# Performance work log

Hardware: AMD Instinct MI355X
Metric: run time of the kernel (lower is better)

Reference implementation:

```python
import jax, jax.numpy as jnp
import numpy as np

EPS = 1e-5
TOP_K = 2


def setup_inputs() -> dict:
    key = jax.random.key(0)
    ks = jax.random.split(key, 6)
    T, H, F, E = 4096, 1024, 2816, 8
    scale = 0.02
    return {
        "hidden_states": jax.random.normal(ks[0], (T, H), dtype=jnp.float32),
        "ln_w": jnp.ones((H,), dtype=jnp.float32),
        "router_w": jax.random.normal(ks[1], (H, E), dtype=jnp.float32) * scale,
        "w_gate": jax.random.normal(ks[2], (E, H, F), dtype=jnp.float32) * scale,
        "w_up": jax.random.normal(ks[3], (E, H, F), dtype=jnp.float32) * scale,
        "w_down": jax.random.normal(ks[4], (E, F, H), dtype=jnp.float32) * scale,
    }


def reference(hidden_states, ln_w, router_w, w_gate, w_up, w_down):
    # RMSNorm (LlamaRMSNorm)
    var = jnp.mean(hidden_states * hidden_states, axis=-1, keepdims=True)
    x = hidden_states * jax.lax.rsqrt(var + EPS) * ln_w  # [T, H]

    # TopKRouter: softmax over experts, then top-k probs/indices
    logits = x @ router_w                     # [T, E]
    probs = jax.nn.softmax(logits, axis=-1)
    topk_p, topk_i = jax.lax.top_k(probs, TOP_K)  # [T, K]

    # Dense combine weights [T, E]: prob for routed experts, 0 otherwise
    T = x.shape[0]
    combine = jnp.zeros_like(probs).at[jnp.arange(T)[:, None], topk_i].add(topk_p)

    # Experts: Llama-style gated MLP (SwiGLU); loop over fixed small expert set
    out = jnp.zeros_like(x)
    for e in range(w_gate.shape[0]):
        h = jax.nn.silu(x @ w_gate[e]) * (x @ w_up[e])   # [T, F]
        out = out + combine[:, e:e + 1] * (h @ w_down[e])
    return out
```

## Files before the change

kernel.cpp:

```cpp
#include <hip/hip_runtime.h>

#define T_TOK 4096
#define H_DIM 1024
#define F_DIM 2816
#define E_NUM 8
#define EPSV 1e-5f

typedef unsigned short u16;
typedef __attribute__((ext_vector_type(8))) short bf16x8;
typedef __attribute__((ext_vector_type(4))) float f32x4;

__device__ __forceinline__ u16 f2bf(float f) {
  union { float f; unsigned u; } c; c.f = f;
  unsigned u = c.u;
  return (u16)((u + 0x7FFFu + ((u >> 16) & 1u)) >> 16);
}

__global__ __launch_bounds__(256) void router_kernel(
    const float* __restrict__ hs, const float* __restrict__ lnw,
    const float* __restrict__ rw, u16* __restrict__ x_h,
    int* __restrict__ cnt, int* __restrict__ list,
    float* __restrict__ wcomb, int* __restrict__ slot) {
  const int wave = threadIdx.x >> 6;
  const int lane = threadIdx.x & 63;
  const int t = blockIdx.x * 4 + wave;
  const float* row = hs + (size_t)t * H_DIM;

  float4 v[4];
  float ss = 0.f;
#pragma unroll
  for (int j = 0; j < 4; ++j) {
    v[j] = ((const float4*)row)[j * 64 + lane];
    ss += v[j].x * v[j].x + v[j].y * v[j].y + v[j].z * v[j].z + v[j].w * v[j].w;
  }
#pragma unroll
  for (int m = 32; m; m >>= 1) ss += __shfl_xor(ss, m, 64);
  const float inv = rsqrtf(ss * (1.0f / H_DIM) + EPSV);

  float lg[E_NUM];
#pragma unroll
  for (int e = 0; e < E_NUM; ++e) lg[e] = 0.f;

#pragma unroll
  for (int j = 0; j < 4; ++j) {
    const int idx = j * 64 + lane;
    const int h0 = idx * 4;
    float4 w4 = ((const float4*)lnw)[idx];
    float xv[4] = {v[j].x * inv * w4.x, v[j].y * inv * w4.y,
                   v[j].z * inv * w4.z, v[j].w * inv * w4.w};
    ushort4 xs;
    xs.x = f2bf(xv[0]); xs.y = f2bf(xv[1]); xs.z = f2bf(xv[2]); xs.w = f2bf(xv[3]);
    ((ushort4*)(x_h + (size_t)t * H_DIM))[idx] = xs;
#pragma unroll
    for (int q = 0; q < 4; ++q) {
      const float* rr = rw + (size_t)(h0 + q) * E_NUM;
      float4 a = ((const float4*)rr)[0];
      float4 b = ((const float4*)rr)[1];
      lg[0] += xv[q] * a.x; lg[1] += xv[q] * a.y;
      lg[2] += xv[q] * a.z; lg[3] += xv[q] * a.w;
      lg[4] += xv[q] * b.x; lg[5] += xv[q] * b.y;
      lg[6] += xv[q] * b.z; lg[7] += xv[q] * b.w;
    }
  }
#pragma unroll
  for (int e = 0; e < E_NUM; ++e)
#pragma unroll
    for (int m = 32; m; m >>= 1) lg[e] += __shfl_xor(lg[e], m, 64);

  if (lane == 0) {
    float mx = lg[0];
#pragma unroll
    for (int e = 1; e < E_NUM; ++e) mx = fmaxf(mx, lg[e]);
    float p[E_NUM], s = 0.f;
#pragma unroll
    for (int e = 0; e < E_NUM; ++e) { p[e] = __expf(lg[e] - mx); s += p[e]; }
    const float invs = 1.0f / s;
    int e1 = 0; float b1 = p[0];
#pragma unroll
    for (int e = 1; e < E_NUM; ++e) if (p[e] > b1) { b1 = p[e]; e1 = e; }
    int e2 = -1; float b2 = -1.f;
#pragma unroll
    for (int e = 0; e < E_NUM; ++e) if (e != e1 && p[e] > b2) { b2 = p[e]; e2 = e; }
    b1 *= invs; b2 *= invs;
    int p1 = atomicAdd(&cnt[e1], 1);
    list[e1 * T_TOK + p1] = t; wcomb[e1 * T_TOK + p1] = b1;
    slot[2 * t] = (e1 << 16) | p1;
    int p2 = atomicAdd(&cnt[e2], 1);
    list[e2 * T_TOK + p2] = t; wcomb[e2 * T_TOK + p2] = b2;
    slot[2 * t + 1] = (e2 << 16) | p2;
  }
}

__global__ void offsets_kernel(const int* __restrict__ cnt, int* __restrict__ offs) {
  if (threadIdx.x == 0) {
    int s = 0;
    for (int e = 0; e < E_NUM; ++e) { offs[e] = s; s += cnt[e]; }
  }
}

__global__ __launch_bounds__(256) void transpose_cvt(
    const float* __restrict__ in, u16* __restrict__ out, int R, int C) {
  __shared__ float tile[32][33];
  const size_t base = (size_t)blockIdx.z * R * C;
  const int c0 = blockIdx.x * 32, r0 = blockIdx.y * 32;
  const int tx = threadIdx.x, ty = threadIdx.y;
#pragma unroll
  for (int j = 0; j < 32; j += 8)
    tile[ty + j][tx] = in[base + (size_t)(r0 + ty + j) * C + c0 + tx];
  __syncthreads();
#pragma unroll
  for (int j = 0; j < 32; j += 8)
    out[base + (size_t)(c0 + ty + j) * R + r0 + tx] = f2bf(tile[tx][ty + j]);
}

__global__ __launch_bounds__(256) void gemm1_kernel(
    const u16* __restrict__ x_h, const u16* __restrict__ wgT,
    const u16* __restrict__ wuT, const int* __restrict__ cnt,
    const int* __restrict__ offs, const int* __restrict__ list,
    u16* __restrict__ hbuf) {
  const int e = blockIdx.z;
  const int n_e = cnt[e];
  const int rt = blockIdx.y;
  if (rt * 128 >= n_e) return;
  const int ft = blockIdx.x;

  __shared__ __align__(16) u16 As[128][72];
  __shared__ __align__(16) u16 Bgs[64][72];
  __shared__ __align__(16) u16 Bus[64][72];
  __shared__ int tok[128];

  const int tid = threadIdx.x;
  if (tid < 128) {
    int r = rt * 128 + tid;
    if (r >= n_e) r = n_e - 1;
    tok[tid] = list[e * T_TOK + r];
  }
  __syncthreads();

  const int wv = tid >> 6, lane = tid & 63;
  const int wm = wv >> 1, wn = wv & 1;
  const int lrow = lane & 15, quad = lane >> 4;

  f32x4 accg[4][2], accu[4][2];
#pragma unroll
  for (int i = 0; i < 4; ++i)
#pragma unroll
    for (int j = 0; j < 2; ++j) {
      accg[i][j] = f32x4{0.f, 0.f, 0.f, 0.f};
      accu[i][j] = f32x4{0.f, 0.f, 0.f, 0.f};
    }

  const size_t wb = ((size_t)e * F_DIM + (size_t)ft * 64) * H_DIM;

  for (int k0 = 0; k0 < H_DIM; k0 += 64) {
#pragma unroll
    for (int i = 0; i < 4; ++i) {
      int c = tid + i * 256;
      int r = c >> 3, kc = (c & 7) << 3;
      *(uint4*)&As[r][kc] = *(const uint4*)(x_h + (size_t)tok[r] * H_DIM + k0 + kc);
    }
#pragma unroll
    for (int i = 0; i < 2; ++i) {
      int c = tid + i * 256;
      int fr = c >> 3, kc = (c & 7) << 3;
      size_t g = wb + (size_t)fr * H_DIM + k0 + kc;
      *(uint4*)&Bgs[fr][kc] = *(const uint4*)(wgT + g);
      *(uint4*)&Bus[fr][kc] = *(const uint4*)(wuT + g);
    }
    __syncthreads();
#pragma unroll
    for (int ks = 0; ks < 2; ++ks) {
      const int kk = ks * 32 + quad * 8;
      bf16x8 a[4], bg[2], bu[2];
#pragma unroll
      for (int tm = 0; tm < 4; ++tm)
        a[tm] = *(const bf16x8*)&As[wm * 64 + tm * 16 + lrow][kk];
#pragma unroll
      for (int tn = 0; tn < 2; ++tn) {
        bg[tn] = *(const bf16x8*)&Bgs[wn * 32 + tn * 16 + lrow][kk];
        bu[tn] = *(const bf16x8*)&Bus[wn * 32 + tn * 16 + lrow][kk];
      }
#pragma unroll
      for (int tm = 0; tm < 4; ++tm)
#pragma unroll
        for (int tn = 0; tn < 2; ++tn) {
          accg[tm][tn] = __builtin_amdgcn_mfma_f32_16x16x32_bf16(a[tm], bg[tn], accg[tm][tn], 0, 0, 0);
          accu[tm][tn] = __builtin_amdgcn_mfma_f32_16x16x32_bf16(a[tm], bu[tn], accu[tm][tn], 0, 0, 0);
        }
    }
    __syncthreads();
  }

  const int oe = offs[e];
#pragma unroll
  for (int tm = 0; tm < 4; ++tm) {
    const int lr0 = wm * 64 + tm * 16 + quad * 4;
#pragma unroll
    for (int rr = 0; rr < 4; ++rr) {
      const int gr = rt * 128 + lr0 + rr;
      if (gr < n_e) {
#pragma unroll
        for (int tn = 0; tn < 2; ++tn) {
          float g = accg[tm][tn][rr];
          float u = accu[tm][tn][rr];
          float hv = g / (1.0f + __expf(-g)) * u;
          int col = ft * 64 + wn * 32 + tn * 16 + lrow;
          hbuf[(size_t)(oe + gr) * F_DIM + col] = f2bf(hv);
        }
      }
    }
  }
}

__global__ __launch_bounds__(256) void gemm2_kernel(
    const u16* __restrict__ hbuf, const u16* __restrict__ wdT,
    const int* __restrict__ cnt, const int* __restrict__ offs,
    const float* __restrict__ wcomb, float* __restrict__ contrib) {
  const int e = blockIdx.z;
  const int n_e = cnt[e];
  const int rt = blockIdx.y;
  if (rt * 128 >= n_e) return;
  const int nt = blockIdx.x;

  __shared__ __align__(16) u16 As[128][72];
  __shared__ __align__(16) u16 Bs[64][72];
  __shared__ int hrow[128];

  const int tid = threadIdx.x;
  const int oe = offs[e];
  if (tid < 128) {
    int r = rt * 128 + tid;
    if (r >= n_e) r = n_e - 1;
    hrow[tid] = oe + r;
  }
  __syncthreads();

  const int wv = tid >> 6, lane = tid & 63;
  const int wm = wv >> 1, wn = wv & 1;
  const int lrow = lane & 15, quad = lane >> 4;

  f32x4 acc[4][2];
#pragma unroll
  for (int i = 0; i < 4; ++i)
#pragma unroll
    for (int j = 0; j < 2; ++j) acc[i][j] = f32x4{0.f, 0.f, 0.f, 0.f};

  const size_t wb = ((size_t)e * H_DIM + (size_t)nt * 64) * F_DIM;

  for (int k0 = 0; k0 < F_DIM; k0 += 64) {
#pragma unroll
    for (int i = 0; i < 4; ++i) {
      int c = tid + i * 256;
      int r = c >> 3, kc = (c & 7) << 3;
      *(uint4*)&As[r][kc] = *(const uint4*)(hbuf + (size_t)hrow[r] * F_DIM + k0 + kc);
    }
#pragma unroll
    for (int i = 0; i < 2; ++i) {
      int c = tid + i * 256;
      int fr = c >> 3, kc = (c & 7) << 3;
      *(uint4*)&Bs[fr][kc] = *(const uint4*)(wdT + wb + (size_t)fr * F_DIM + k0 + kc);
    }
    __syncthreads();
#pragma unroll
    for (int ks = 0; ks < 2; ++ks) {
      const int kk = ks * 32 + quad * 8;
      bf16x8 a[4], b[2];
#pragma unroll
      for (int tm = 0; tm < 4; ++tm)
        a[tm] = *(const bf16x8*)&As[wm * 64 + tm * 16 + lrow][kk];
#pragma unroll
      for (int tn = 0; tn < 2; ++tn)
        b[tn] = *(const bf16x8*)&Bs[wn * 32 + tn * 16 + lrow][kk];
#pragma unroll
      for (int tm = 0; tm < 4; ++tm)
#pragma unroll
        for (int tn = 0; tn < 2; ++tn)
          acc[tm][tn] = __builtin_amdgcn_mfma_f32_16x16x32_bf16(a[tm], b[tn], acc[tm][tn], 0, 0, 0);
    }
    __syncthreads();
  }

#pragma unroll
  for (int tm = 0; tm < 4; ++tm) {
    const int lr0 = wm * 64 + tm * 16 + quad * 4;
#pragma unroll
    for (int rr = 0; rr < 4; ++rr) {
      const int gr = rt * 128 + lr0 + rr;
      if (gr < n_e) {
        const float cw = wcomb[e * T_TOK + gr];
#pragma unroll
        for (int tn = 0; tn < 2; ++tn) {
          int col = nt * 64 + wn * 32 + tn * 16 + lrow;
          contrib[(size_t)(oe + gr) * H_DIM + col] = acc[tm][tn][rr] * cw;
        }
      }
    }
  }
}

__global__ __launch_bounds__(256) void combine_kernel(
    const float* __restrict__ contrib, const int* __restrict__ offs,
    const int* __restrict__ slot, float* __restrict__ out) {
  const int t = blockIdx.x;
  const int s0 = slot[2 * t], s1 = slot[2 * t + 1];
  const int r0 = offs[s0 >> 16] + (s0 & 0xFFFF);
  const int r1 = offs[s1 >> 16] + (s1 & 0xFFFF);
  float4 a = ((const float4*)(contrib + (size_t)r0 * H_DIM))[threadIdx.x];
  float4 b = ((const float4*)(contrib + (size_t)r1 * H_DIM))[threadIdx.x];
  float4 o = {a.x + b.x, a.y + b.y, a.z + b.z, a.w + b.w};
  ((float4*)(out + (size_t)t * H_DIM))[threadIdx.x] = o;
}

extern "C" void kernel_launch(void* const* d_in, const int* in_sizes, int n_in,
                              void* d_out, int out_size, void* d_ws, size_t ws_size,
                              hipStream_t stream) {
  const float* hs  = (const float*)d_in[0];
  const float* lnw = (const float*)d_in[1];
  const float* rw  = (const float*)d_in[2];
  const float* wg  = (const float*)d_in[3];
  const float* wu  = (const float*)d_in[4];
  const float* wd  = (const float*)d_in[5];
  float* out = (float*)d_out;

  char* p = (char*)d_ws;
  const size_t SZ_XH = (size_t)T_TOK * H_DIM * 2;
  const size_t SZ_W  = (size_t)E_NUM * F_DIM * H_DIM * 2;
  const size_t SZ_HB = (size_t)T_TOK * 2 * F_DIM * 2;
  const size_t SZ_CT = (size_t)T_TOK * 2 * H_DIM * 4;

  u16* x_h  = (u16*)p;   p += SZ_XH;
  u16* wgT  = (u16*)p;   p += SZ_W;
  u16* wuT  = (u16*)p;   p += SZ_W;
  u16* wdT  = (u16*)p;   p += SZ_W;
  u16* hbuf = (u16*)p;   p += SZ_HB;
  float* contrib = (float*)p; p += SZ_CT;
  int* cnt  = (int*)p;   p += 256;
  int* offs = (int*)p;   p += 256;
  int* list = (int*)p;   p += (size_t)E_NUM * T_TOK * 4;
  float* wcomb = (float*)p; p += (size_t)E_NUM * T_TOK * 4;
  int* slot = (int*)p;   p += (size_t)T_TOK * 2 * 4;

  hipMemsetAsync(cnt, 0, 256, stream);
  router_kernel<<<T_TOK / 4, 256, 0, stream>>>(hs, lnw, rw, x_h, cnt, list, wcomb, slot);
  offsets_kernel<<<1, 64, 0, stream>>>(cnt, offs);
  transpose_cvt<<<dim3(F_DIM / 32, H_DIM / 32, E_NUM), dim3(32, 8), 0, stream>>>(wg, wgT, H_DIM, F_DIM);
  transpose_cvt<<<dim3(F_DIM / 32, H_DIM / 32, E_NUM), dim3(32, 8), 0, stream>>>(wu, wuT, H_DIM, F_DIM);
  transpose_cvt<<<dim3(H_DIM / 32, F_DIM / 32, E_NUM), dim3(32, 8), 0, stream>>>(wd, wdT, F_DIM, H_DIM);
  gemm1_kernel<<<dim3(F_DIM / 64, T_TOK / 128, E_NUM), 256, 0, stream>>>(x_h, wgT, wuT, cnt, offs, list, hbuf);
  gemm2_kernel<<<dim3(H_DIM / 64, T_TOK / 128, E_NUM), 256, 0, stream>>>(hbuf, wdT, cnt, offs, wcomb, contrib);
  combine_kernel<<<T_TOK, 256, 0, stream>>>(contrib, offs, slot, out);
}
```

Before: 673.6 us.

## Use direct global-to-LDS loads with XOR swizzle and widen gemm2 N tile

Result: faster. 654.4 us (-2.9%).

```diff
diff --git a/kernel.cpp b/kernel.cpp
--- a/kernel.cpp
+++ b/kernel.cpp
@@ -14,6 +14,12 @@
   union { float f; unsigned u; } c; c.f = f;
   unsigned u = c.u;
   return (u16)((u + 0x7FFFu + ((u >> 16) & 1u)) >> 16);
+}
+
+__device__ __forceinline__ void llds16(const u16* g, u16* l) {
+  __builtin_amdgcn_global_load_lds(
+      (const __attribute__((address_space(1))) unsigned int*)g,
+      (__attribute__((address_space(3))) unsigned int*)l, 16, 0, 0);
 }
 
 __global__ __launch_bounds__(256) void router_kernel(
@@ -124,9 +130,9 @@
   if (rt * 128 >= n_e) return;
   const int ft = blockIdx.x;
 
-  __shared__ __align__(16) u16 As[128][72];
-  __shared__ __align__(16) u16 Bgs[64][72];
-  __shared__ __align__(16) u16 Bus[64][72];
+  __shared__ __align__(16) u16 As[128 * 64];
+  __shared__ __align__(16) u16 Bgs[64 * 64];
+  __shared__ __align__(16) u16 Bus[64 * 64];
   __shared__ int tok[128];
 
   const int tid = threadIdx.x;
@@ -140,6 +146,42 @@
   const int wv = tid >> 6, lane = tid & 63;
   const int wm = wv >> 1, wn = wv & 1;
   const int lrow = lane & 15, quad = lane >> 4;
+  const int srow = lane >> 3, schunk = lane & 7;
+
+  const u16* agp[4];
+#pragma unroll
+  for (int i = 0; i < 4; ++i) {
+    int r = wv * 32 + i * 8 + srow;
+    agp[i] = x_h + (size_t)tok[r] * H_DIM + ((schunk ^ (r & 7)) << 3);
+  }
+  const size_t wb = ((size_t)e * F_DIM + (size_t)ft * 64) * H_DIM;
+  const u16* bgp[2]; const u16* bup[2];
+#pragma unroll
+  for (int i = 0; i < 2; ++i) {
+    int r = wv * 16 + i * 8 + srow;
+    size_t g = wb + (size_t)r * H_DIM + ((schunk ^ (r & 7)) << 3);
+    bgp[i] = wgT + g;
+    bup[i] = wuT + g;
+  }
+
+  const u16* aptr[4][2]; const u16* bgptr[2][2]; const u16* buptr[2][2];
+#pragma unroll
+  for (int tm = 0; tm < 4; ++tm) {
+    int row = wm * 64 + tm * 16 + lrow;
+#pragma unroll
+    for (int ks = 0; ks < 2; ++ks)
+      aptr[tm][ks] = &As[row * 64 + (((ks * 4 + quad) ^ (row & 7)) << 3)];
+  }
+#pragma unroll
+  for (int tn = 0; tn < 2; ++tn) {
+    int row = wn * 32 + tn * 16 + lrow;
+#pragma unroll
+    for (int ks = 0; ks < 2; ++ks) {
+      int off = row * 64 + (((ks * 4 + quad) ^ (row & 7)) << 3);
+      bgptr[tn][ks] = &Bgs[off];
+      buptr[tn][ks] = &Bus[off];
+    }
+  }
 
   f32x4 accg[4][2], accu[4][2];
 #pragma unroll
@@ -150,35 +192,25 @@
       accu[i][j] = f32x4{0.f, 0.f, 0.f, 0.f};
     }
 
-  const size_t wb = ((size_t)e * F_DIM + (size_t)ft * 64) * H_DIM;
-
   for (int k0 = 0; k0 < H_DIM; k0 += 64) {
 #pragma unroll
-    for (int i = 0; i < 4; ++i) {
-      int c = tid + i * 256;
-      int r = c >> 3, kc = (c & 7) << 3;
-      *(uint4*)&As[r][kc] = *(const uint4*)(x_h + (size_t)tok[r] * H_DIM + k0 + kc);
-    }
+    for (int i = 0; i < 4; ++i)
+      llds16(agp[i] + k0, &As[(wv * 32 + i * 8) * 64]);
 #pragma unroll
     for (int i = 0; i < 2; ++i) {
-      int c = tid + i * 256;
-      int fr = c >> 3, kc = (c & 7) << 3;
-      size_t g = wb + (size_t)fr * H_DIM + k0 + kc;
-      *(uint4*)&Bgs[fr][kc] = *(const uint4*)(wgT + g);
-      *(uint4*)&Bus[fr][kc] = *(const uint4*)(wuT + g);
+      llds16(bgp[i] + k0, &Bgs[(wv * 16 + i * 8) * 64]);
+      llds16(bup[i] + k0, &Bus[(wv * 16 + i * 8) * 64]);
     }
     __syncthreads();
 #pragma unroll
     for (int ks = 0; ks < 2; ++ks) {
-      const int kk = ks * 32 + quad * 8;
       bf16x8 a[4], bg[2], bu[2];
 #pragma unroll
-      for (int tm = 0; tm < 4; ++tm)
-        a[tm] = *(const bf16x8*)&As[wm * 64 + tm * 16 + lrow][kk];
+      for (int tm = 0; tm < 4; ++tm) a[tm] = *(const bf16x8*)aptr[tm][ks];
 #pragma unroll
       for (int tn = 0; tn < 2; ++tn) {
-        bg[tn] = *(const bf16x8*)&Bgs[wn * 32 + tn * 16 + lrow][kk];
-        bu[tn] = *(const bf16x8*)&Bus[wn * 32 + tn * 16 + lrow][kk];
+        bg[tn] = *(const bf16x8*)bgptr[tn][ks];
+        bu[tn] = *(const bf16x8*)buptr[tn][ks];
       }
 #pragma unroll
       for (int tm = 0; tm < 4; ++tm)
@@ -222,8 +254,8 @@
   if (rt * 128 >= n_e) return;
   const int nt = blockIdx.x;
 
-  __shared__ __align__(16) u16 As[128][72];
-  __shared__ __align__(16) u16 Bs[64][72];
+  __shared__ __align__(16) u16 As[128 * 64];
+  __shared__ __align__(16) u16 Bs[128 * 64];
   __shared__ int hrow[128];
 
   const int tid = threadIdx.x;
@@ -238,43 +270,62 @@
   const int wv = tid >> 6, lane = tid & 63;
   const int wm = wv >> 1, wn = wv & 1;
   const int lrow = lane & 15, quad = lane >> 4;
-
-  f32x4 acc[4][2];
+  const int srow = lane >> 3, schunk = lane & 7;
+
+  const u16* agp[4];
+#pragma unroll
+  for (int i = 0; i < 4; ++i) {
+    int r = wv * 32 + i * 8 + srow;
+    agp[i] = hbuf + (size_t)hrow[r] * F_DIM + ((schunk ^ (r & 7)) << 3);
+  }
+  const size_t wb = ((size_t)e * H_DIM + (size_t)nt * 128) * F_DIM;
+  const u16* bgp[4];
+#pragma unroll
+  for (int i = 0; i < 4; ++i) {
+    int r = wv * 32 + i * 8 + srow;
+    bgp[i] = wdT + wb + (size_t)r * F_DIM + ((schunk ^ (r & 7)) << 3);
+  }
+
+  const u16* aptr[4][2]; const u16* bptr[4][2];
+#pragma unroll
+  for (int tm = 0; tm < 4; ++tm) {
+    int row = wm * 64 + tm * 16 + lrow;
+#pragma unroll
+    for (int ks = 0; ks < 2; ++ks)
+      aptr[tm][ks] = &As[row * 64 + (((ks * 4 + quad) ^ (row & 7)) << 3)];
+  }
+#pragma unroll
+  for (int tn = 0; tn < 4; ++tn) {
+    int row = wn * 64 + tn * 16 + lrow;
+#pragma unroll
+    for (int ks = 0; ks < 2; ++ks)
+      bptr[tn][ks] = &Bs[row * 64 + (((ks * 4 + quad) ^ (row & 7)) << 3)];
+  }
+
+  f32x4 acc[4][4];
 #pragma unroll
   for (int i = 0; i < 4; ++i)
 #pragma unroll
-    for (int j = 0; j < 2; ++j) acc[i][j] = f32x4{0.f, 0.f, 0.f, 0.f};
-
-  const size_t wb = ((size_t)e * H_DIM + (size_t)nt * 64) * F_DIM;
+    for (int j = 0; j < 4; ++j) acc[i][j] = f32x4{0.f, 0.f, 0.f, 0.f};
 
   for (int k0 = 0; k0 < F_DIM; k0 += 64) {
 #pragma unroll
     for (int i = 0; i < 4; ++i) {
-      int c = tid + i * 256;
-      int r = c >> 3, kc = (c & 7) << 3;
-      *(uint4*)&As[r][kc] = *(const uint4*)(hbuf + (size_t)hrow[r] * F_DIM + k0 + kc);
-    }
-#pragma unroll
-    for (int i = 0; i < 2; ++i) {
-      int c = tid + i * 256;
-      int fr = c >> 3, kc = (c & 7) << 3;
-      *(uint4*)&Bs[fr][kc] = *(const uint4*)(wdT + wb + (size_t)fr * F_DIM + k0 + kc);
+      llds16(agp[i] + k0, &As[(wv * 32 + i * 8) * 64]);
+      llds16(bgp[i] + k0, &Bs[(wv * 32 + i * 8) * 64]);
     }
     __syncthreads();
 #pragma unroll
     for (int ks = 0; ks < 2; ++ks) {
-      const int kk = ks * 32 + quad * 8;
-      bf16x8 a[4], b[2];
+      bf16x8 a[4], b[4];
+#pragma unroll
+      for (int tm = 0; tm < 4; ++tm) a[tm] = *(const bf16x8*)aptr[tm][ks];
+#pragma unroll
+      for (int tn = 0; tn < 4; ++tn) b[tn] = *(const bf16x8*)bptr[tn][ks];
 #pragma unroll
       for (int tm = 0; tm < 4; ++tm)
-        a[tm] = *(const bf16x8*)&As[wm * 64 + tm * 16 + lrow][kk];
-#pragma unroll
-      for (int tn = 0; tn < 2; ++tn)
-        b[tn] = *(const bf16x8*)&Bs[wn * 32 + tn * 16 + lrow][kk];
-#pragma unroll
-      for (int tm = 0; tm < 4; ++tm)
-#pragma unroll
-        for (int tn = 0; tn < 2; ++tn)
+#pragma unroll
+        for (int tn = 0; tn < 4; ++tn)
           acc[tm][tn] = __builtin_amdgcn_mfma_f32_16x16x32_bf16(a[tm], b[tn], acc[tm][tn], 0, 0, 0);
     }
     __syncthreads();
@@ -289,8 +340,8 @@
       if (gr < n_e) {
         const float cw = wcomb[e * T_TOK + gr];
 #pragma unroll
-        for (int tn = 0; tn < 2; ++tn) {
-          int col = nt * 64 + wn * 32 + tn * 16 + lrow;
+        for (int tn = 0; tn < 4; ++tn) {
+          int col = nt * 128 + wn * 64 + tn * 16 + lrow;
           contrib[(size_t)(oe + gr) * H_DIM + col] = acc[tm][tn][rr] * cw;
         }
       }
@@ -347,6 +398,6 @@
   transpose_cvt<<<dim3(F_DIM / 32, H_DIM / 32, E_NUM), dim3(32, 8), 0, stream>>>(wu, wuT, H_DIM, F_DIM);
   transpose_cvt<<<dim3(H_DIM / 32, F_DIM / 32, E_NUM), dim3(32, 8), 0, stream>>>(wd, wdT, F_DIM, H_DIM);
   gemm1_kernel<<<dim3(F_DIM / 64, T_TOK / 128, E_NUM), 256, 0, stream>>>(x_h, wgT, wuT, cnt, offs, list, hbuf);
-  gemm2_kernel<<<dim3(H_DIM / 64, T_TOK / 128, E_NUM), 256, 0, stream>>>(hbuf, wdT, cnt, offs, wcomb, contrib);
+  gemm2_kernel<<<dim3(H_DIM / 128, T_TOK / 128, E_NUM), 256, 0, stream>>>(hbuf, wdT, cnt, offs, wcomb, contrib);
   combine_kernel<<<T_TOK, 256, 0, stream>>>(contrib, offs, slot, out);
 }
```
